# Kernel tuning notes

Measured on AMD Instinct MI355X. Metric: run time of the kernel, lower is better.

## Reference

```python
import jax, jax.numpy as jnp
import numpy as np

NUM_HEADS = 16
HEAD_DIM = 64
EMBED_DIM = 1024
MASKED_BIAS = -10000.0


def setup_inputs() -> dict:
    key = jax.random.key(0)
    ks = jax.random.split(key, 4)
    B, S, D = 4, 1024, EMBED_DIM
    scale = 0.02
    return {
        "hidden_states": jax.random.normal(ks[0], (B, S, D), dtype=jnp.float32),
        "c_attn_w": jax.random.normal(ks[1], (D, 3 * D), dtype=jnp.float32) * scale,
        "c_attn_b": jnp.zeros((3 * D,), dtype=jnp.float32),
        "c_proj_w": jax.random.normal(ks[2], (D, D), dtype=jnp.float32) * scale,
        "c_proj_b": jnp.zeros((D,), dtype=jnp.float32),
        "affine_w": jnp.ones((D,), dtype=jnp.float32),
        "affine_b": jnp.zeros((D,), dtype=jnp.float32),
    }


def reference(hidden_states, c_attn_w, c_attn_b, c_proj_w, c_proj_b, affine_w, affine_b):
    B, S, D = hidden_states.shape
    H, Dh = NUM_HEADS, HEAD_DIM
    # c_attn (GPT2 Conv1D): x @ W + b -> [B,S,3D], split into q,k,v
    qkv = hidden_states @ c_attn_w + c_attn_b
    q, k, v = jnp.split(qkv, 3, axis=-1)
    # split heads -> [B,H,S,Dh]
    def split_heads(t):
        return t.reshape(B, S, H, Dh).transpose(0, 2, 1, 3)
    q, k, v = split_heads(q), split_heads(k), split_heads(v)
    # QK^T scaled by 1/sqrt(head_dim) (value.size(-1)**0.5)
    attn_weights = jnp.einsum("bhqd,bhkd->bhqk", q, k) / jnp.asarray(
        Dh, hidden_states.dtype) ** 0.5
    # causal mask via where with -10000 sentinel (eager GPT2 semantics)
    causal = jnp.tril(jnp.ones((S, S), dtype=bool))[None, None]
    attn_weights = jnp.where(causal, attn_weights,
                             jnp.asarray(MASKED_BIAS, attn_weights.dtype))
    attn_weights = jax.nn.softmax(attn_weights, axis=-1)
    # attn dropout = identity in eval
    attn_output = jnp.einsum("bhqk,bhkd->bhqd", attn_weights, v)
    # merge heads -> [B,S,D]
    attn_output = attn_output.transpose(0, 2, 1, 3).reshape(B, S, D)
    # c_proj (Conv1D), resid dropout identity, then affine
    attn_output = attn_output @ c_proj_w + c_proj_b
    attn_output = attn_output * affine_w + affine_b
    return attn_output
```

## Files before the change

### kernel.cpp

```cpp
#include <hip/hip_runtime.h>


typedef __attribute__((ext_vector_type(4))) float  fx4;
typedef __attribute__((ext_vector_type(4))) short  sx4;
typedef __attribute__((ext_vector_type(8))) short  sx8;
typedef __attribute__((ext_vector_type(4))) float  f32x4;
typedef __attribute__((ext_vector_type(8))) __bf16 bf16x8;

#define DEVI static __device__ __forceinline__

DEVI short f2bf(float f) {
  unsigned u = __builtin_bit_cast(unsigned, f);
  u = (u + 0x7FFFu + ((u >> 16) & 1u)) >> 16;
  return (short)u;
}

DEVI fx4 mfma16(sx8 a, sx8 b, fx4 c) {
  return __builtin_amdgcn_mfma_f32_16x16x32_bf16(
      __builtin_bit_cast(bf16x8, a), __builtin_bit_cast(bf16x8, b), c, 0, 0, 0);
}

DEVI void gl_lds16(const void* g, void* l) {
  __builtin_amdgcn_global_load_lds(
      (const __attribute__((address_space(1))) void*)g,
      (__attribute__((address_space(3))) void*)l, 16, 0, 0);
}

__global__ __launch_bounds__(256) void cast_bf16(const float* __restrict__ in,
                                                 short* __restrict__ out, int n4) {
  int i = blockIdx.x * blockDim.x + threadIdx.x;
  if (i < n4) {
    f32x4 v = *(const f32x4*)&in[(size_t)i * 4];
    sx4 o;
#pragma unroll
    for (int j = 0; j < 4; ++j) o[j] = f2bf(v[j]);
    *(sx4*)&out[(size_t)i * 4] = o;
  }
}

__global__ __launch_bounds__(256) void transpose_bf16(const float* __restrict__ in,
                                                      short* __restrict__ out,
                                                      int R, int C) {
  __shared__ float t[32][33];
  int tx = threadIdx.x & 31, ty = threadIdx.x >> 5;
  int r0 = blockIdx.y * 32, c0 = blockIdx.x * 32;
#pragma unroll
  for (int i = 0; i < 4; ++i)
    t[ty + i * 8][tx] = in[(size_t)(r0 + ty + i * 8) * C + c0 + tx];
  __syncthreads();
#pragma unroll
  for (int i = 0; i < 4; ++i)
    out[(size_t)(c0 + ty + i * 8) * R + r0 + tx] = f2bf(t[tx][ty + i * 8]);
}

template <int EPI>
__global__ __launch_bounds__(256) void gemm_bt(
    const short* __restrict__ A, const short* __restrict__ Bt,
    const float* __restrict__ bias, const float* __restrict__ aw,
    const float* __restrict__ ab, short* __restrict__ Qg, short* __restrict__ Kg,
    short* __restrict__ Vtg, float* __restrict__ Out, int M, int N, int K) {
  __shared__ __align__(16) short As[128][64];
  __shared__ __align__(16) short Bs[128][64];
  const int tid = threadIdx.x, lane = tid & 63, w = tid >> 6;
  const int bn = blockIdx.x, bm = blockIdx.y;
  const int wm = w >> 1, wn = w & 1;
  const int c0 = lane & 15, g = lane >> 4;
  const int lr8 = lane >> 3;
  const int ls8 = (lane & 7) ^ lr8;
  fx4 acc[4][4] = {};

  for (int kt = 0; kt < K; kt += 64) {
#pragma unroll
    for (int i = 0; i < 4; ++i) {
      int r = w * 32 + i * 8;
      gl_lds16(&A[(size_t)(bm * 128 + r + lr8) * K + kt + ls8 * 8], &As[r][0]);
      gl_lds16(&Bt[(size_t)(bn * 128 + r + lr8) * K + kt + ls8 * 8], &Bs[r][0]);
    }
    __syncthreads();
#pragma unroll
    for (int kk = 0; kk < 2; ++kk) {
      sx8 af[4], bf[4];
      int sb = kk * 4 + g;
#pragma unroll
      for (int m = 0; m < 4; ++m) {
        int row = wm * 64 + m * 16 + c0;
        af[m] = *(const sx8*)&As[row][(sb ^ (row & 7)) * 8];
      }
#pragma unroll
      for (int n = 0; n < 4; ++n) {
        int row = wn * 64 + n * 16 + c0;
        bf[n] = *(const sx8*)&Bs[row][(sb ^ (row & 7)) * 8];
      }
#pragma unroll
      for (int m = 0; m < 4; ++m)
#pragma unroll
        for (int n = 0; n < 4; ++n) acc[m][n] = mfma16(af[m], bf[n], acc[m][n]);
    }
    __syncthreads();
  }

  const float SCALE_Q = 0.125f * 1.4426950408889634f;
#pragma unroll
  for (int m = 0; m < 4; ++m) {
#pragma unroll
    for (int n = 0; n < 4; ++n) {
      int col = bn * 128 + wn * 64 + n * 16 + c0;
      int row0 = bm * 128 + wm * 64 + m * 16 + g * 4;
      if (EPI == 0) {
        float bv = bias[col];
        int b = row0 >> 10, s0 = row0 & 1023;
        if (col < 1024) {
          int h = col >> 6, d = col & 63;
          size_t base = ((size_t)(b * 16 + h) * 1024) * 64 + d;
#pragma unroll
          for (int r = 0; r < 4; ++r)
            Qg[base + (size_t)(s0 + r) * 64] = f2bf((acc[m][n][r] + bv) * SCALE_Q);
        } else if (col < 2048) {
          int c = col - 1024, h = c >> 6, d = c & 63;
          size_t base = ((size_t)(b * 16 + h) * 1024) * 64 + d;
#pragma unroll
          for (int r = 0; r < 4; ++r)
            Kg[base + (size_t)(s0 + r) * 64] = f2bf(acc[m][n][r] + bv);
        } else {
          int c = col - 2048, h = c >> 6, d = c & 63;
          sx4 v;
#pragma unroll
          for (int r = 0; r < 4; ++r) v[r] = f2bf(acc[m][n][r] + bv);
          *(sx4*)&Vtg[((size_t)(b * 16 + h) * 64 + d) * 1024 + s0] = v;
        }
      } else {
        float bv = bias[col], wv = aw[col], av = ab[col];
#pragma unroll
        for (int r = 0; r < 4; ++r)
          Out[(size_t)(row0 + r) * N + col] = (acc[m][n][r] + bv) * wv + av;
      }
    }
  }
}

__global__ __launch_bounds__(256, 4) void attn_kernel(const short* __restrict__ Qg,
                                                      const short* __restrict__ Kg,
                                                      const short* __restrict__ Vtg,
                                                      short* __restrict__ AO) {
  __shared__ __align__(16) short Ks[2][64][64];
  __shared__ __align__(16) short Vts[2][64][64];
  __shared__ __align__(16) short Ps[4][16 * 64];
  const int tid = threadIdx.x, lane = tid & 63, w = tid >> 6;
  const int bid = blockIdx.x;
  const int u = bid >> 8, v = bid & 255, bh = v >> 2, jj = v & 3;
  const int qt = (u == 0) ? jj : (u == 1) ? 7 - jj : (u == 2) ? 8 + jj : 15 - jj;
  const int b = bh >> 4, h = bh & 15;
  const int c0 = lane & 15, g = lane >> 4;
  const int lr8 = lane >> 3, ls8 = (lane & 7) ^ lr8;
  const int q0 = qt * 64 + w * 16;
  const short* Qp = Qg + (size_t)bh * 65536;
  const short* Kp = Kg + (size_t)bh * 65536;
  const short* Vp = Vtg + (size_t)bh * 65536;
  short* pbase = &Ps[w][0];
  const int s8 = (c0 & 7) * 8;

  sx8 qf[2];
#pragma unroll
  for (int kk = 0; kk < 2; ++kk)
    qf[kk] = *(const sx8*)&Qp[(size_t)(q0 + c0) * 64 + kk * 32 + g * 8];

  fx4 o[4] = {};
  float mrun = -1e30f, lrun = 0.f;
  const int q_glob = q0 + c0;

  auto STAGE = [&](int bf, int kv0) {
#pragma unroll
    for (int i = 0; i < 2; ++i) {
      int idx = w * 2 + i;
      gl_lds16(&Kp[(size_t)(kv0 + idx * 8 + lr8) * 64 + ls8 * 8], &Ks[bf][idx * 8][0]);
    }
#pragma unroll
    for (int i = 0; i < 2; ++i) {
      int idx = w * 2 + i;
      gl_lds16(&Vp[(size_t)(idx * 8 + lr8) * 1024 + kv0 + ls8 * 8], &Vts[bf][idx * 8][0]);
    }
  };

  STAGE(0, 0);
  for (int t = 0; t <= qt; ++t) {
    const int kv0 = t * 64;
    const int bf = t & 1;
    const bool more = t < qt;
    if (more) {
      STAGE(bf ^ 1, kv0 + 64);
      asm volatile("s_waitcnt vmcnt(4)" ::: "memory");
    } else {
      asm volatile("s_waitcnt vmcnt(0)" ::: "memory");
    }
    __builtin_amdgcn_s_barrier();

    fx4 st[4];
    __builtin_amdgcn_s_setprio(1);
#pragma unroll
    for (int mf = 0; mf < 4; ++mf) {
      int row = mf * 16 + c0;
      sx8 kf0 = *(const sx8*)&Ks[bf][row][(g ^ (row & 7)) * 8];
      sx8 kf1 = *(const sx8*)&Ks[bf][row][((4 + g) ^ (row & 7)) * 8];
      fx4 z = {0.f, 0.f, 0.f, 0.f};
      z = mfma16(kf0, qf[0], z);
      st[mf] = mfma16(kf1, qf[1], z);
    }
    __builtin_amdgcn_s_setprio(0);

    float pmax = -1e30f;
    if (t == qt) {
#pragma unroll
      for (int mf = 0; mf < 4; ++mf)
#pragma unroll
        for (int r = 0; r < 4; ++r) {
          int kv = kv0 + mf * 16 + g * 4 + r;
          float z = (kv > q_glob) ? -1e30f : st[mf][r];
          st[mf][r] = z;
          pmax = fmaxf(pmax, z);
        }
    } else {
#pragma unroll
      for (int mf = 0; mf < 4; ++mf)
#pragma unroll
        for (int r = 0; r < 4; ++r) pmax = fmaxf(pmax, st[mf][r]);
    }
    pmax = fmaxf(pmax, __shfl_xor(pmax, 16));
    pmax = fmaxf(pmax, __shfl_xor(pmax, 32));
    float mnew = fmaxf(mrun, pmax);
    float alpha = __builtin_amdgcn_exp2f(mrun - mnew);
    float psum = 0.f;
#pragma unroll
    for (int mf = 0; mf < 4; ++mf) {
      sx4 pv;
#pragma unroll
      for (int r = 0; r < 4; ++r) {
        float pp = __builtin_amdgcn_exp2f(st[mf][r] - mnew);
        psum += pp;
        pv[r] = f2bf(pp);
      }
      *(sx4*)&pbase[c0 * 64 + ((mf * 16 + g * 4) ^ s8)] = pv;
    }
    psum += __shfl_xor(psum, 16);
    psum += __shfl_xor(psum, 32);
    lrun = lrun * alpha + psum;
    mrun = mnew;
#pragma unroll
    for (int mf = 0; mf < 4; ++mf) o[mf] *= alpha;

    __builtin_amdgcn_s_setprio(1);
#pragma unroll
    for (int kk = 0; kk < 2; ++kk) {
      sx8 pbf = *(const sx8*)&pbase[c0 * 64 + ((kk * 32 + g * 8) ^ s8)];
#pragma unroll
      for (int mf = 0; mf < 4; ++mf) {
        int row = mf * 16 + c0;
        sx8 vaf = *(const sx8*)&Vts[bf][row][((kk * 4 + g) ^ (row & 7)) * 8];
        o[mf] = mfma16(vaf, pbf, o[mf]);
      }
    }
    __builtin_amdgcn_s_setprio(0);
    __builtin_amdgcn_s_barrier();
  }

  float inv = 1.0f / lrun;
  int q = q0 + c0;
#pragma unroll
  for (int mf = 0; mf < 4; ++mf) {
    sx4 v4;
#pragma unroll
    for (int r = 0; r < 4; ++r) v4[r] = f2bf(o[mf][r] * inv);
    int d0 = mf * 16 + g * 4;
    *(sx4*)&AO[((size_t)(b * 1024 + q)) * 1024 + h * 64 + d0] = v4;
  }
}

extern "C" void kernel_launch(void* const* d_in, const int* in_sizes, int n_in,
                              void* d_out, int out_size, void* d_ws, size_t ws_size,
                              hipStream_t stream) {
  const float* hs  = (const float*)d_in[0];
  const float* caw = (const float*)d_in[1];
  const float* cab = (const float*)d_in[2];
  const float* cpw = (const float*)d_in[3];
  const float* cpb = (const float*)d_in[4];
  const float* afw = (const float*)d_in[5];
  const float* afb = (const float*)d_in[6];
  float* out = (float*)d_out;
  char* ws = (char*)d_ws;

  short* hsb    = (short*)(ws);
  short* ao     = (short*)(ws);
  short* wqkvt  = (short*)(ws + ((size_t)8  << 20));
  short* wprojt = (short*)(ws + ((size_t)14 << 20));
  short* Qg     = (short*)(ws + ((size_t)16 << 20));
  short* Kg     = (short*)(ws + ((size_t)24 << 20));
  short* Vtg    = (short*)(ws + ((size_t)32 << 20));

  cast_bf16<<<4096, 256, 0, stream>>>(hs, hsb, 1048576);
  transpose_bf16<<<dim3(96, 32), 256, 0, stream>>>(caw, wqkvt, 1024, 3072);
  transpose_bf16<<<dim3(32, 32), 256, 0, stream>>>(cpw, wprojt, 1024, 1024);
  gemm_bt<0><<<dim3(24, 32), 256, 0, stream>>>(hsb, wqkvt, cab, nullptr, nullptr,
                                               Qg, Kg, Vtg, nullptr, 4096, 3072, 1024);
  attn_kernel<<<1024, 256, 0, stream>>>(Qg, Kg, Vtg, ao);
  gemm_bt<1><<<dim3(8, 32), 256, 0, stream>>>(ao, wprojt, cpb, afw, afb,
                                              nullptr, nullptr, nullptr, out, 4096, 1024, 1024);
}
```

Before: 100.8 us.

## Double-buffer LDS tiles in GEMM to overlap global loads with MFMA

```diff
diff --git a/kernel.cpp b/kernel.cpp
--- a/kernel.cpp
+++ b/kernel.cpp
@@ -54,13 +54,13 @@
 }
 
 template <int EPI>
-__global__ __launch_bounds__(256) void gemm_bt(
+__global__ __launch_bounds__(256, 2) void gemm_bt(
     const short* __restrict__ A, const short* __restrict__ Bt,
     const float* __restrict__ bias, const float* __restrict__ aw,
     const float* __restrict__ ab, short* __restrict__ Qg, short* __restrict__ Kg,
     short* __restrict__ Vtg, float* __restrict__ Out, int M, int N, int K) {
-  __shared__ __align__(16) short As[128][64];
-  __shared__ __align__(16) short Bs[128][64];
+  __shared__ __align__(16) short As[2][128][64];
+  __shared__ __align__(16) short Bs[2][128][64];
   const int tid = threadIdx.x, lane = tid & 63, w = tid >> 6;
   const int bn = blockIdx.x, bm = blockIdx.y;
   const int wm = w >> 1, wn = w & 1;
@@ -68,35 +68,47 @@
   const int lr8 = lane >> 3;
   const int ls8 = (lane & 7) ^ lr8;
   fx4 acc[4][4] = {};
-
-  for (int kt = 0; kt < K; kt += 64) {
+  const int nkt = K >> 6;
+
+  auto STAGE = [&](int bf, int kt) {
 #pragma unroll
     for (int i = 0; i < 4; ++i) {
       int r = w * 32 + i * 8;
-      gl_lds16(&A[(size_t)(bm * 128 + r + lr8) * K + kt + ls8 * 8], &As[r][0]);
-      gl_lds16(&Bt[(size_t)(bn * 128 + r + lr8) * K + kt + ls8 * 8], &Bs[r][0]);
-    }
-    __syncthreads();
+      gl_lds16(&A[(size_t)(bm * 128 + r + lr8) * K + kt + ls8 * 8], &As[bf][r][0]);
+      gl_lds16(&Bt[(size_t)(bn * 128 + r + lr8) * K + kt + ls8 * 8], &Bs[bf][r][0]);
+    }
+  };
+
+  STAGE(0, 0);
+  for (int t = 0; t < nkt; ++t) {
+    const int bf = t & 1;
+    if (t + 1 < nkt) {
+      STAGE(bf ^ 1, (t + 1) * 64);
+      asm volatile("s_waitcnt vmcnt(8)" ::: "memory");
+    } else {
+      asm volatile("s_waitcnt vmcnt(0)" ::: "memory");
+    }
+    __builtin_amdgcn_s_barrier();
 #pragma unroll
     for (int kk = 0; kk < 2; ++kk) {
-      sx8 af[4], bf[4];
+      sx8 af[4], bfr[4];
       int sb = kk * 4 + g;
 #pragma unroll
       for (int m = 0; m < 4; ++m) {
         int row = wm * 64 + m * 16 + c0;
-        af[m] = *(const sx8*)&As[row][(sb ^ (row & 7)) * 8];
+        af[m] = *(const sx8*)&As[bf][row][(sb ^ (row & 7)) * 8];
       }
 #pragma unroll
       for (int n = 0; n < 4; ++n) {
         int row = wn * 64 + n * 16 + c0;
-        bf[n] = *(const sx8*)&Bs[row][(sb ^ (row & 7)) * 8];
+        bfr[n] = *(const sx8*)&Bs[bf][row][(sb ^ (row & 7)) * 8];
       }
 #pragma unroll
       for (int m = 0; m < 4; ++m)
 #pragma unroll
-        for (int n = 0; n < 4; ++n) acc[m][n] = mfma16(af[m], bf[n], acc[m][n]);
-    }
-    __syncthreads();
+        for (int n = 0; n < 4; ++n) acc[m][n] = mfma16(af[m], bfr[n], acc[m][n]);
+    }
+    __builtin_amdgcn_s_barrier();
   }
 
   const float SCALE_Q = 0.125f * 1.4426950408889634f;
```

New measurement: 104.7 us. 1.04x slower.
